# Kernel tuning notes

Hardware: AMD Instinct MI355X
Metric: run time of the kernel (lower is better)

## Reference

```python
import jax, jax.numpy as jnp
import numpy as np

B, NE, NN, L = 64, 256, 1024, 512
F_IN, HID = 128, 128
VOCAB = 50000
ALPHA = 0.2
NEG = -9.0e15


def _leaky(z):
    return jnp.where(z >= 0, z, ALPHA * z)


def hga_layer(x, adj, W, W2, W3, a, a2, wc, transfer, concat):
    # x: [B, NN, Fin], adj: [B, NE, NN] (hyperedge incidence)
    O = W2.shape[1]
    x4 = x @ W2                      # [B, NN, O]
    if transfer:
        x = x @ W                    # [B, NN, O]
    # node->edge attention: score depends only on node k (query is shared word_context)
    s0 = wc[0] @ a[:O, 0]            # scalar
    e1 = _leaky(x4 @ a[O:, 0] + s0)  # [B, NN]
    e1 = jnp.broadcast_to(e1[:, None, :], adj.shape)          # [B, NE, NN]
    att_edge = jax.nn.softmax(jnp.where(adj > 0, e1, NEG), axis=2)
    edge = att_edge @ x              # [B, NE, O]
    edge4 = edge @ W3                # [B, NE, O]
    # edge->node attention: query = node feat x4[k], key = edge feat edge4[j]
    e2 = _leaky((x4 @ a2[:O, 0])[:, None, :] + (edge4 @ a2[O:, 0])[:, :, None])  # [B, NE, NN]
    att_node = jax.nn.softmax(jnp.where(adj > 0, e2, NEG).transpose(0, 2, 1), axis=2)  # [B, NN, NE]
    node = att_node @ edge           # [B, NN, O]
    return jax.nn.elu(node) if concat else node


def setup_inputs() -> dict:
    key = jax.random.key(0)
    ks = jax.random.split(key, 16)
    stdv = 1.0 / np.sqrt(HID)
    u = lambda k, shape: jax.random.uniform(k, shape, jnp.float32, -stdv, stdv)
    inp = {
        "items": jax.random.randint(ks[0], (B, NN), 0, VOCAB),
        "alias_inputs": jax.random.randint(ks[1], (B, L), 0, NN),
        "node_masks": jnp.ones((B, L), jnp.float32),
        "adj": jax.random.randint(ks[2], (B, NE, NN), 0, 2).astype(jnp.float32),
        "emb": jax.random.normal(ks[3], (VOCAB, F_IN), jnp.float32),
        # layer 1 (transfer=False, concat=True)
        "w2_1": u(ks[4], (F_IN, HID)),
        "w3_1": u(ks[5], (HID, HID)),
        "a_1": u(ks[6], (2 * HID, 1)),
        "a2_1": u(ks[7], (2 * HID, 1)),
        "wc_1": u(ks[8], (1, HID)),
        # layer 2 (transfer=True, concat=False)
        "w_2": u(ks[9], (HID, HID)),
        "w2_2": u(ks[10], (HID, HID)),
        "w3_2": u(ks[11], (HID, HID)),
        "a_2": u(ks[12], (2 * HID, 1)),
        "a2_2": u(ks[13], (2 * HID, 1)),
        "wc_2": u(ks[14], (1, HID)),
        "ln_g": jnp.ones((HID,), jnp.float32),
        "ln_b": jnp.zeros((HID,), jnp.float32),
    }
    return inp


def reference(items, alias_inputs, node_masks, adj, emb,
              w2_1, w3_1, a_1, a2_1, wc_1,
              w_2, w2_2, w3_2, a_2, a2_2, wc_2,
              ln_g, ln_b):
    hidden = emb[items]                                        # [B, NN, F]
    x = hga_layer(hidden, adj, None, w2_1, w3_1, a_1, a2_1, wc_1,
                  transfer=False, concat=True)
    x = hga_layer(x, adj, w_2, w2_2, w3_2, a_2, a2_2, wc_2,
                  transfer=True, concat=False)                 # [B, NN, HID]
    seq = jnp.take_along_axis(x, alias_inputs[:, :, None], axis=1)  # [B, L, HID]
    m = node_masks[:, :, None]
    h = seq * m
    b = jnp.sum(h * m, axis=-2) / jnp.sum(node_masks, -1, keepdims=True)  # [B, HID]
    mu = jnp.mean(b, -1, keepdims=True)
    var = jnp.mean((b - mu) ** 2, -1, keepdims=True)
    return (b - mu) / jnp.sqrt(var + 1e-6) * ln_g + ln_b
```

## Files before the change

kernel.cpp:

```cpp
#include <hip/hip_runtime.h>
#include <hip/hip_bf16.h>

typedef __hip_bfloat16 bf16;
typedef __attribute__((ext_vector_type(8))) unsigned short u16x8;
typedef __attribute__((ext_vector_type(4))) unsigned short u16x4;
typedef __attribute__((ext_vector_type(4))) float f32x4;
typedef __attribute__((ext_vector_type(8))) short bf16x8;

#define B_   64
#define NE_  256
#define NN_  1024
#define L_   512
#define HID_ 128
#define ALPHA_ 0.2f

__device__ __forceinline__ float bfu(unsigned short u){
  unsigned int x = ((unsigned int)u) << 16;
  union { unsigned int i; float f; } c; c.i = x; return c.f;
}
__device__ __forceinline__ unsigned short f2b(float f){
  bf16 h = __float2bfloat16(f);
  union { bf16 b; unsigned short u; } c; c.b = h; return c.u;
}
__device__ __forceinline__ int swz(int r, int c){ return (c ^ (r & 3) ^ ((r >> 2) & 3)) & 3; }

__global__ void k_small(const float* __restrict__ w2_1, const float* __restrict__ w3_1,
                        const float* __restrict__ a_1,  const float* __restrict__ a2_1,
                        const float* __restrict__ wc_1,
                        const float* __restrict__ w2_2, const float* __restrict__ w3_2,
                        const float* __restrict__ a_2,  const float* __restrict__ a2_2,
                        const float* __restrict__ wc_2,
                        const float* __restrict__ w_2,
                        const int* __restrict__ alias, const float* __restrict__ masks,
                        float* __restrict__ consts, unsigned short* __restrict__ W2T,
                        float* __restrict__ wcount, float* __restrict__ msum,
                        float* __restrict__ pooled)
{
  __shared__ float wcs[1024];
  __shared__ float red4[4];
  int blk = blockIdx.x, t = threadIdx.x;
  if (blk < 6) {
    if (t < 128) {
      const float* M; const float* v;
      switch (blk) {
        case 0: M = w2_1; v = a_1  + 128; break;
        case 1: M = w2_1; v = a2_1;       break;
        case 2: M = w3_1; v = a2_1 + 128; break;
        case 3: M = w2_2; v = a_2  + 128; break;
        case 4: M = w2_2; v = a2_2;       break;
        default: M = w3_2; v = a2_2 + 128; break;
      }
      float acc = 0.f;
      #pragma unroll 4
      for (int o = 0; o < 128; o += 4) {
        f32x4 m = *(const f32x4*)(M + t*128 + o);
        f32x4 x = *(const f32x4*)(v + o);
        acc += m[0]*x[0] + m[1]*x[1] + m[2]*x[2] + m[3]*x[3];
      }
      consts[blk*128 + t] = acc;
    }
  } else if (blk < 8) {
    const float* wc = (blk == 6) ? wc_1 : wc_2;
    const float* a  = (blk == 6) ? a_1  : a_2;
    if (t < 64) {
      float s = wc[t]*a[t] + wc[t+64]*a[t+64];
      #pragma unroll
      for (int sh = 32; sh > 0; sh >>= 1) s += __shfl_xor(s, sh);
      if (t == 0) consts[768 + (blk - 6)] = s;
    }
  } else if (blk == 8) {
    if (t < 128) for (int k = 0; k < 128; ++k) W2T[t*128 + k] = f2b(w_2[k*128 + t]);
  } else if (blk == 9) {
    for (int i = t; i < B_*HID_; i += 256) pooled[i] = 0.f;
  } else {
    int b = blk - 10;
    #pragma unroll
    for (int j = 0; j < 4; ++j) wcs[t + j*256] = 0.f;
    __syncthreads();
    float s = 0.f;
    #pragma unroll
    for (int j = 0; j < 2; ++j) {
      int l = t + j*256;
      float m = masks[b*L_ + l];
      int idx = alias[b*L_ + l];
      atomicAdd(&wcs[idx], m*m);
      s += m;
    }
    #pragma unroll
    for (int sh = 32; sh > 0; sh >>= 1) s += __shfl_xor(s, sh);
    if ((t & 63) == 0) red4[t >> 6] = s;
    __syncthreads();
    if (t == 0) msum[b] = red4[0] + red4[1] + red4[2] + red4[3];
    #pragma unroll
    for (int j = 0; j < 4; ++j) wcount[(long)b*NN_ + t + j*256] = wcs[t + j*256];
  }
}

__global__ __launch_bounds__(256) void k_prep(
    const float* __restrict__ adj,
    unsigned long long* __restrict__ ADJBb,
    unsigned short* __restrict__ ADJT16)
{
  __shared__ unsigned long long Lbits[16][17];
  const int id = blockIdx.x;
  const int b  = id & 63;
  const int ec = id >> 6;
  const int t  = threadIdx.x;
  const int wv = t >> 6, lane = t & 63;
  const int grp = lane >> 4;
  const int gl  = lane & 15;

  #pragma unroll
  for (int rr = 0; rr < 4; ++rr) {
    const int r = wv*4 + rr;
    const int e = ec*16 + r;
    const float* src = adj + ((long)b*NE_ + e)*NN_;
    #pragma unroll
    for (int i = 0; i < 4; ++i) {
      f32x4 v = *(const f32x4*)(src + i*256 + lane*4);
      unsigned long long nib =
            (unsigned long long)(v[0] != 0.f)
          | ((unsigned long long)(v[1] != 0.f) << 1)
          | ((unsigned long long)(v[2] != 0.f) << 2)
          | ((unsigned long long)(v[3] != 0.f) << 3);
      unsigned long long word = nib << (gl * 4);
      #pragma unroll
      for (int s = 1; s < 16; s <<= 1)
        word |= __shfl_xor(word, s);
      if (gl == 0) {
        Lbits[r][i*4 + grp] = word;
        ADJBb[((long)b*NE_ + e)*16 + i*4 + grp] = word;
      }
    }
  }
  __syncthreads();
  #pragma unroll
  for (int j = 0; j < 4; ++j) {
    int n = t + 256*j;
    int w = n >> 6, bitn = n & 63;
    unsigned int o = 0;
    #pragma unroll
    for (int rr = 0; rr < 16; ++rr)
      o |= (unsigned int)((Lbits[rr][w] >> bitn) & 1ull) << rr;
    ADJT16[((long)b*NN_ + n)*16 + ec] = (unsigned short)o;
  }
}

__global__ void k_fproj(const float* __restrict__ emb, const int* __restrict__ gitems,
                        const float* __restrict__ consts,
                        float* __restrict__ w1, float* __restrict__ f1,
                        unsigned short* __restrict__ YT)
{
  __shared__ float ce1s[128], cf1s[128];
  __shared__ __attribute__((aligned(16))) unsigned short T[64][132];
  int b = blockIdx.y, n0 = blockIdx.x * 64, t = threadIdx.x;
  if (t < 128) { ce1s[t] = consts[t]; cf1s[t] = consts[128 + t]; }
  __syncthreads();
  int r = t >> 2, h0 = (t & 3) * 32;
  long row = (long)b*NN_ + n0 + r;
  float s0 = consts[768];
  float xv[32];
  const float* sp = emb + (long)gitems[row]*HID_ + h0;
  #pragma unroll
  for (int j = 0; j < 32; j += 4) {
    f32x4 v = *(const f32x4*)(sp + j);
    #pragma unroll
    for (int k = 0; k < 4; ++k) xv[j+k] = v[k];
  }
  float p1 = 0.f, p2 = 0.f;
  #pragma unroll
  for (int j = 0; j < 32; ++j) { p1 += xv[j]*ce1s[h0+j]; p2 += xv[j]*cf1s[h0+j]; }
  p1 += __shfl_xor(p1, 1, 4); p1 += __shfl_xor(p1, 2, 4);
  p2 += __shfl_xor(p2, 1, 4); p2 += __shfl_xor(p2, 2, 4);
  float z = p1 + s0; z = (z >= 0.f) ? z : ALPHA_*z;
  float w = __expf(z);
  if ((t & 3) == 0) { w1[row] = w; f1[row] = p2; }
  #pragma unroll
  for (int j = 0; j < 32; j += 4) {
    u16x4 o;
    #pragma unroll
    for (int k = 0; k < 4; ++k) o[k] = f2b(w * xv[j+k]);
    *(u16x4*)&T[r][h0+j] = o;
  }
  __syncthreads();
  int h = t >> 1, nh = (t & 1) * 32;
  unsigned short* dst = YT + ((long)b*HID_ + h)*NN_ + n0 + nh;
  #pragma unroll
  for (int j = 0; j < 32; j += 8) {
    u16x8 o;
    #pragma unroll
    for (int k = 0; k < 8; ++k) o[k] = T[nh+j+k][h];
    *(u16x8*)&dst[j] = o;
  }
}

template<int TRANSFER>
__global__ __launch_bounds__(256) void k_gemm_edge(
    const unsigned char* __restrict__ ADJ8,
    const unsigned short* __restrict__ YT,
    const float* __restrict__ w1v,
    const float* __restrict__ consts, int layer,
    const unsigned short* __restrict__ W2T,
    unsigned short* __restrict__ ET,
    float* __restrict__ f2o)
{
  __shared__ __attribute__((aligned(16))) unsigned short SM[12288];
  __shared__ float dsum[64];
  const int id = blockIdx.x;
  const int b = id & 63;
  const long e0 = (long)(id >> 6) * 64;
  const int t = threadIdx.x;
  const int lane = t & 63;
  const int w = t >> 6, wm = w >> 1, wn = w & 1;
  const int r4 = t >> 2, c4 = t & 3;
  const int lr = lane & 15, g = lane >> 4;

  f32x4 acc[2][4];
  #pragma unroll
  for (int i = 0; i < 2; ++i)
    #pragma unroll
    for (int j = 0; j < 4; ++j) acc[i][j] = (f32x4){0.f,0.f,0.f,0.f};

  const unsigned char*  Ab = ADJ8 + ((long)b*NE_ + e0 + r4)*(NN_ >> 3);
  const unsigned short* Bb = YT + (long)b*HID_*NN_;
  const float*          wb = w1v + (long)b*NN_;

  unsigned int ab; u16x8 bv0, bv1; f32x4 wv0, wv1;
  float dot = 0.f;

  auto stage = [&](int kc) {
    ab  = Ab[(kc >> 3) + c4];
    wv0 = *(const f32x4*)(wb + kc + c4*8);
    wv1 = *(const f32x4*)(wb + kc + c4*8 + 4);
    bv0 = *(const u16x8*)(Bb + (long)r4*NN_ + kc + c4*8);
    bv1 = *(const u16x8*)(Bb + (long)(64+r4)*NN_ + kc + c4*8);
  };
  auto commit = [&](int buf) {
    u16x8 av;
    #pragma unroll
    for (int j = 0; j < 8; ++j) {
      unsigned int bit = (ab >> j) & 1u;
      av[j] = bit ? (unsigned short)0x3F80 : (unsigned short)0;
      float wj = (j < 4) ? wv0[j] : wv1[j-4];
      dot += bit ? wj : 0.f;
    }
    *(u16x8*)&SM[buf*2048 + r4*32 + swz(r4,c4)*8] = av;
    *(u16x8*)&SM[4096 + buf*4096 + r4*32 + swz(r4,c4)*8] = bv0;
    *(u16x8*)&SM[4096 + buf*4096 + (64+r4)*32 + swz(64+r4,c4)*8] = bv1;
  };

  stage(0); commit(0);
  int cur = 0;
  const int NIT = NN_/32;
  for (int it = 0; it < NIT; ++it) {
    __syncthreads();
    if (it+1 < NIT) stage((it+1)*32);
    const unsigned short* AsB = &SM[cur*2048];
    const unsigned short* BsB = &SM[4096 + cur*4096];
    bf16x8 af[2], bfr[4];
    #pragma unroll
    for (int mt = 0; mt < 2; ++mt) {
      int r = wm*32 + mt*16 + lr;
      af[mt] = *(const bf16x8*)&AsB[r*32 + swz(r,g)*8];
    }
    #pragma unroll
    for (int nt = 0; nt < 4; ++nt) {
      int n = wn*64 + nt*16 + lr;
      bfr[nt] = *(const bf16x8*)&BsB[n*32 + swz(n,g)*8];
    }
    #pragma unroll
    for (int mt = 0; mt < 2; ++mt)
      #pragma unroll
      for (int nt = 0; nt < 4; ++nt)
        acc[mt][nt] = __builtin_amdgcn_mfma_f32_16x16x32_bf16(af[mt], bfr[nt], acc[mt][nt], 0, 0, 0);
    if (it+1 < NIT) { commit(cur^1); cur ^= 1; }
  }
  dot += __shfl_down(dot, 2, 4); dot += __shfl_down(dot, 1, 4);
  if ((lane & 3) == 0) dsum[r4] = dot;
  __syncthreads();
  #pragma unroll
  for (int mt = 0; mt < 2; ++mt)
    #pragma unroll
    for (int nt = 0; nt < 4; ++nt) {
      int col = wn*64 + nt*16 + lr;
      #pragma unroll
      for (int q = 0; q < 4; ++q) {
        int rl = wm*32 + mt*16 + g*4 + q;
        SM[rl*136 + col] = f2b(acc[mt][nt][q] / dsum[rl]);
      }
    }
  __syncthreads();
  if (TRANSFER) {
    f32x4 acc2[2][4];
    #pragma unroll
    for (int i = 0; i < 2; ++i)
      #pragma unroll
      for (int j = 0; j < 4; ++j) acc2[i][j] = (f32x4){0.f,0.f,0.f,0.f};
    #pragma unroll
    for (int kc2 = 0; kc2 < 4; ++kc2) {
      bf16x8 af[2], bfr[4];
      #pragma unroll
      for (int mt = 0; mt < 2; ++mt) {
        int r = wm*32 + mt*16 + lr;
        af[mt] = *(const bf16x8*)&SM[r*136 + kc2*32 + g*8];
      }
      #pragma unroll
      for (int nt = 0; nt < 4; ++nt) {
        int n = wn*64 + nt*16 + lr;
        bfr[nt] = *(const bf16x8*)(W2T + n*128 + kc2*32 + g*8);
      }
      #pragma unroll
      for (int mt = 0; mt < 2; ++mt)
        #pragma unroll
        for (int nt = 0; nt < 4; ++nt)
          acc2[mt][nt] = __builtin_amdgcn_mfma_f32_16x16x32_bf16(af[mt], bfr[nt], acc2[mt][nt], 0, 0, 0);
    }
    __syncthreads();
    #pragma unroll
    for (int mt = 0; mt < 2; ++mt)
      #pragma unroll
      for (int nt = 0; nt < 4; ++nt) {
        int col = wn*64 + nt*16 + lr;
        #pragma unroll
        for (int q = 0; q < 4; ++q) {
          int rl = wm*32 + mt*16 + g*4 + q;
          SM[rl*136 + col] = f2b(acc2[mt][nt][q]);
        }
      }
    __syncthreads();
  }
  {
    const float* cf2 = consts + layer*384 + 256;
    int r = t >> 2, h0 = (t & 3) * 32;
    float p = 0.f;
    #pragma unroll
    for (int j = 0; j < 32; ++j) p += bfu(SM[r*136 + h0 + j]) * cf2[h0 + j];
    p += __shfl_down(p, 2, 4); p += __shfl_down(p, 1, 4);
    if ((t & 3) == 0) f2o[(long)b*NE_ + e0 + r] = p;
  }
  {
    int h = t >> 1, eh = (t & 1) * 32;
    unsigned short* dst = ET + ((long)b*HID_ + h)*NE_ + e0 + eh;
    #pragma unroll
    for (int j = 0; j < 32; j += 8) {
      u16x8 o;
      #pragma unroll
      for (int k = 0; k < 8; ++k) o[k] = SM[(eh+j+k)*136 + h];
      *(u16x8*)&dst[j] = o;
    }
  }
}

template<int EPI>
__global__ __launch_bounds__(256, 2) void k_gemm_att(
    const unsigned char* __restrict__ ADJ8,
    const unsigned short* __restrict__ ET,
    const float* __restrict__ f1v, const float* __restrict__ f2v,
    const float* __restrict__ consts,
    unsigned short* __restrict__ YTout, float* __restrict__ w1o, float* __restrict__ f1o,
    const float* __restrict__ wcount, float* __restrict__ pooled)
{
  __shared__ __attribute__((aligned(16))) unsigned short SM[12288];
  __shared__ float dsum[64];
  __shared__ float colsum[128];
  __shared__ float wrow[64];
  const int id = blockIdx.x;
  const int b = id & 63;
  const long m0 = (long)(id >> 6) * 64;
  const int t = threadIdx.x;
  const int lane = t & 63;
  const int w = t >> 6, wm = w >> 1, wn = w & 1;
  const int r4 = t >> 2, c4 = t & 3;
  const int lr = lane & 15, g = lane >> 4;

  f32x4 acc[2][4];
  #pragma unroll
  for (int i = 0; i < 2; ++i)
    #pragma unroll
    for (int j = 0; j < 4; ++j) acc[i][j] = (f32x4){0.f,0.f,0.f,0.f};

  const float f1r = f1v[(long)b*NN_ + m0 + r4];
  const unsigned char*  Ab = ADJ8 + ((long)b*NN_ + m0 + r4)*(NE_ >> 3);
  const unsigned short* Bb = ET + (long)b*HID_*NE_;
  const float* f2p = f2v + (long)b*NE_;

  unsigned int ab; u16x8 bv0, bv1; f32x4 fv0, fv1;
  float dot = 0.f;

  auto stage = [&](int kc) {
    ab  = Ab[(kc >> 3) + c4];
    fv0 = *(const f32x4*)(f2p + kc + c4*8);
    fv1 = *(const f32x4*)(f2p + kc + c4*8 + 4);
    bv0 = *(const u16x8*)(Bb + (long)r4*NE_ + kc + c4*8);
    bv1 = *(const u16x8*)(Bb + (long)(64+r4)*NE_ + kc + c4*8);
  };
  auto commit = [&](int buf) {
    u16x8 av;
    #pragma unroll
    for (int j = 0; j < 8; ++j) {
      unsigned int bit = (ab >> j) & 1u;
      float z = f1r + ((j < 4) ? fv0[j] : fv1[j-4]);
      z = (z >= 0.f) ? z : ALPHA_ * z;
      float wt = bit ? __expf(z) : 0.f;
      unsigned short us = f2b(wt);
      av[j] = us; dot += bfu(us);
    }
    *(u16x8*)&SM[buf*2048 + r4*32 + swz(r4,c4)*8] = av;
    *(u16x8*)&SM[4096 + buf*4096 + r4*32 + swz(r4,c4)*8] = bv0;
    *(u16x8*)&SM[4096 + buf*4096 + (64+r4)*32 + swz(64+r4,c4)*8] = bv1;
  };

  stage(0); commit(0);
  int cur = 0;
  const int NIT = NE_/32;
  for (int it = 0; it < NIT; ++it) {
    __syncthreads();
    if (it+1 < NIT) stage((it+1)*32);
    const unsigned short* AsB = &SM[cur*2048];
    const unsigned short* BsB = &SM[4096 + cur*4096];
    bf16x8 af[2], bfr[4];
    #pragma unroll
    for (int mt = 0; mt < 2; ++mt) {
      int r = wm*32 + mt*16 + lr;
      af[mt] = *(const bf16x8*)&AsB[r*32 + swz(r,g)*8];
    }
    #pragma unroll
    for (int nt = 0; nt < 4; ++nt) {
      int n = wn*64 + nt*16 + lr;
      bfr[nt] = *(const bf16x8*)&BsB[n*32 + swz(n,g)*8];
    }
    #pragma unroll
    for (int mt = 0; mt < 2; ++mt)
      #pragma unroll
      for (int nt = 0; nt < 4; ++nt)
        acc[mt][nt] = __builtin_amdgcn_mfma_f32_16x16x32_bf16(af[mt], bfr[nt], acc[mt][nt], 0, 0, 0);
    if (it+1 < NIT) { commit(cur^1); cur ^= 1; }
  }
  dot += __shfl_down(dot, 2, 4); dot += __shfl_down(dot, 1, 4);
  if ((lane & 3) == 0) dsum[r4] = dot;
  if (EPI == 2 && t < 128) colsum[t] = 0.f;
  __syncthreads();

  if (EPI == 1) {
    #pragma unroll
    for (int mt = 0; mt < 2; ++mt)
      #pragma unroll
      for (int nt = 0; nt < 4; ++nt) {
        int col = wn*64 + nt*16 + lr;
        #pragma unroll
        for (int q = 0; q < 4; ++q) {
          int rl = wm*32 + mt*16 + g*4 + q;
          float v = acc[mt][nt][q] / dsum[rl];
          v = (v > 0.f) ? v : expm1f(v);
          SM[rl*136 + col] = f2b(v);
        }
      }
    __syncthreads();
    {
      const float* ce1 = consts + 384;
      const float* cf1 = consts + 512;
      int r = t >> 2, h0 = (t & 3) * 32;
      float p1 = 0.f, p2 = 0.f;
      #pragma unroll
      for (int j = 0; j < 32; ++j) {
        float xv = bfu(SM[r*136 + h0 + j]);
        p1 += xv * ce1[h0 + j];
        p2 += xv * cf1[h0 + j];
      }
      p1 += __shfl_down(p1, 2, 4); p1 += __shfl_down(p1, 1, 4);
      p2 += __shfl_down(p2, 2, 4); p2 += __shfl_down(p2, 1, 4);
      if ((t & 3) == 0) {
        float z = p1 + consts[769];
        z = (z >= 0.f) ? z : ALPHA_ * z;
        float wv = __expf(z);
        wrow[r] = wv;
        w1o[(long)b*NN_ + m0 + r] = wv;
        f1o[(long)b*NN_ + m0 + r] = p2;
      }
    }
    __syncthreads();
    {
      int h = t >> 1, nh = (t & 1) * 32;
      unsigned short* dst = YTout + ((long)b*HID_ + h)*NN_ + m0 + nh;
      #pragma unroll
      for (int j = 0; j < 32; j += 8) {
        u16x8 o;
        #pragma unroll
        for (int k = 0; k < 8; ++k) {
          int rr = nh + j + k;
          o[k] = f2b(wrow[rr] * bfu(SM[rr*136 + h]));
        }
        *(u16x8*)&dst[j] = o;
      }
    }
  } else {
    float psum[4] = {0.f, 0.f, 0.f, 0.f};
    #pragma unroll
    for (int mt = 0; mt < 2; ++mt)
      #pragma unroll
      for (int q = 0; q < 4; ++q) {
        int rl = wm*32 + mt*16 + g*4 + q;
        float wc = wcount[(long)b*NN_ + m0 + rl];
        float inv = wc / dsum[rl];
        #pragma unroll
        for (int nt = 0; nt < 4; ++nt) psum[nt] += inv * acc[mt][nt][q];
      }
    #pragma unroll
    for (int nt = 0; nt < 4; ++nt) atomicAdd(&colsum[wn*64 + nt*16 + lr], psum[nt]);
    __syncthreads();
    if (t < 128) atomicAdd(&pooled[(long)b*HID_ + t], colsum[t]);
  }
}

__global__ void k_ln(const float* __restrict__ pooled, const float* __restrict__ msum,
                     const float* __restrict__ ln_g, const float* __restrict__ ln_b,
                     float* __restrict__ out)
{
  int b = blockIdx.x, t = threadIdx.x;
  __shared__ float sr[2];
  float bv = pooled[b*HID_ + t] / msum[b];
  int lane = t & 63;
  float p = bv;
  #pragma unroll
  for (int s = 32; s > 0; s >>= 1) p += __shfl_xor(p, s);
  if (lane == 0) sr[t >> 6] = p;
  __syncthreads();
  float mu = (sr[0] + sr[1]) * (1.f / HID_);
  float dv = bv - mu;
  p = dv * dv;
  #pragma unroll
  for (int s = 32; s > 0; s >>= 1) p += __shfl_xor(p, s);
  __syncthreads();
  if (lane == 0) sr[t >> 6] = p;
  __syncthreads();
  float var = (sr[0] + sr[1]) * (1.f / HID_);
  out[b*HID_ + t] = dv / sqrtf(var + 1e-6f) * ln_g[t] + ln_b[t];
}

extern "C" void kernel_launch(void* const* d_in, const int* in_sizes, int n_in,
                              void* d_out, int out_size, void* d_ws, size_t ws_size,
                              hipStream_t stream)
{
  const int*   items = (const int*)d_in[0];
  const int*   alias = (const int*)d_in[1];
  const float* masks = (const float*)d_in[2];
  const float* adj   = (const float*)d_in[3];
  const float* emb   = (const float*)d_in[4];
  const float* w2_1  = (const float*)d_in[5];
  const float* w3_1  = (const float*)d_in[6];
  const float* a_1   = (const float*)d_in[7];
  const float* a2_1  = (const float*)d_in[8];
  const float* wc_1  = (const float*)d_in[9];
  const float* w_2   = (const float*)d_in[10];
  const float* w2_2  = (const float*)d_in[11];
  const float* w3_2  = (const float*)d_in[12];
  const float* a_2   = (const float*)d_in[13];
  const float* a2_2  = (const float*)d_in[14];
  const float* wc_2  = (const float*)d_in[15];
  const float* ln_g  = (const float*)d_in[16];
  const float* ln_b  = (const float*)d_in[17];
  float* out = (float*)d_out;

  char* ws = (char*)d_ws;
  size_t off = 0;
  auto alloc = [&](size_t bytes) -> void* {
    void* p = ws + off; off += (bytes + 255) / 256 * 256; return p;
  };
  unsigned long long* ADJBb = (unsigned long long*)alloc((size_t)B_*NE_*(NN_/8));
  unsigned short*     ADJT16= (unsigned short*)    alloc((size_t)B_*NN_*(NE_/8));
  unsigned short* YT   = (unsigned short*)alloc((size_t)B_*HID_*NN_*2);
  unsigned short* ET   = (unsigned short*)alloc((size_t)B_*HID_*NE_*2);
  float* wcount= (float*)alloc((size_t)B_*NN_*4);
  float* pooled= (float*)alloc((size_t)B_*HID_*4);
  float* w1L1  = (float*)alloc((size_t)B_*NN_*4);
  float* f1L1  = (float*)alloc((size_t)B_*NN_*4);
  float* w1L2  = (float*)alloc((size_t)B_*NN_*4);
  float* f1L2  = (float*)alloc((size_t)B_*NN_*4);
  float* f2    = (float*)alloc((size_t)B_*NE_*4);
  float* msum  = (float*)alloc(B_*4);
  float* consts= (float*)alloc(772*4);
  unsigned short* W2T = (unsigned short*)alloc((size_t)HID_*HID_*2);
  if (off > ws_size) return;

  k_small<<<74, 256, 0, stream>>>(w2_1, w3_1, a_1, a2_1, wc_1, w2_2, w3_2, a_2, a2_2, wc_2,
                                  w_2, alias, masks, consts, W2T, wcount, msum, pooled);
  k_prep<<<B_*16, 256, 0, stream>>>(adj, ADJBb, ADJT16);
  k_fproj<<<dim3(NN_/64, B_), 256, 0, stream>>>(emb, items, consts, w1L1, f1L1, YT);

  k_gemm_edge<0><<<B_*(NE_/64), 256, 0, stream>>>((const unsigned char*)ADJBb, YT, w1L1,
        consts, 0, W2T, ET, f2);
  k_gemm_att<1><<<B_*(NN_/64), 256, 0, stream>>>((const unsigned char*)ADJT16, ET, f1L1, f2,
        consts, YT, w1L2, f1L2, nullptr, nullptr);

  k_gemm_edge<1><<<B_*(NE_/64), 256, 0, stream>>>((const unsigned char*)ADJBb, YT, w1L2,
        consts, 1, W2T, ET, f2);
  k_gemm_att<2><<<B_*(NN_/64), 256, 0, stream>>>((const unsigned char*)ADJT16, ET, f1L2, f2,
        consts, nullptr, nullptr, nullptr, wcount, pooled);

  k_ln<<<B_, HID_, 0, stream>>>(pooled, msum, ln_g, ln_b, out);
}
```

Measured before the change: 129.4 us.

## Merge front-end kernels into one launch and fuse layernorm into last attention kernel

Combines the small-constants, adjacency bit-packing and first-layer feature projection kernels into a single grid. The projection blocks recompute the projection constants locally, so they no longer depend on the constants kernel. The final layernorm kernel is removed: the last block finishing each batch row in the final attention kernel, found through an atomic counter, performs the normalization. This cuts two kernel launches and the inter-kernel gaps, at the cost of redundant per-block constant computation and a threadfence plus atomic per block.

```diff
diff --git a/kernel.cpp b/kernel.cpp
--- a/kernel.cpp
+++ b/kernel.cpp
@@ -24,173 +24,192 @@
 }
 __device__ __forceinline__ int swz(int r, int c){ return (c ^ (r & 3) ^ ((r >> 2) & 3)) & 3; }
 
-__global__ void k_small(const float* __restrict__ w2_1, const float* __restrict__ w3_1,
-                        const float* __restrict__ a_1,  const float* __restrict__ a2_1,
-                        const float* __restrict__ wc_1,
-                        const float* __restrict__ w2_2, const float* __restrict__ w3_2,
-                        const float* __restrict__ a_2,  const float* __restrict__ a2_2,
-                        const float* __restrict__ wc_2,
-                        const float* __restrict__ w_2,
-                        const int* __restrict__ alias, const float* __restrict__ masks,
-                        float* __restrict__ consts, unsigned short* __restrict__ W2T,
-                        float* __restrict__ wcount, float* __restrict__ msum,
-                        float* __restrict__ pooled)
+__global__ __launch_bounds__(256) void k_front(
+    const float* __restrict__ adj,
+    unsigned long long* __restrict__ ADJBb, unsigned short* __restrict__ ADJT16,
+    const float* __restrict__ emb, const int* __restrict__ items,
+    const float* __restrict__ w2_1, const float* __restrict__ w3_1,
+    const float* __restrict__ a_1,  const float* __restrict__ a2_1,
+    const float* __restrict__ wc_1,
+    const float* __restrict__ w_2,
+    const float* __restrict__ w2_2, const float* __restrict__ w3_2,
+    const float* __restrict__ a_2,  const float* __restrict__ a2_2,
+    const float* __restrict__ wc_2,
+    const int* __restrict__ alias, const float* __restrict__ masks,
+    float* __restrict__ w1L1, float* __restrict__ f1L1,
+    unsigned short* __restrict__ YT,
+    float* __restrict__ consts, unsigned short* __restrict__ W2T,
+    float* __restrict__ wcount, float* __restrict__ msum,
+    float* __restrict__ pooled, int* __restrict__ lncnt)
 {
-  __shared__ float wcs[1024];
-  __shared__ float red4[4];
-  int blk = blockIdx.x, t = threadIdx.x;
-  if (blk < 6) {
-    if (t < 128) {
-      const float* M; const float* v;
-      switch (blk) {
-        case 0: M = w2_1; v = a_1  + 128; break;
-        case 1: M = w2_1; v = a2_1;       break;
-        case 2: M = w3_1; v = a2_1 + 128; break;
-        case 3: M = w2_2; v = a_2  + 128; break;
-        case 4: M = w2_2; v = a2_2;       break;
-        default: M = w3_2; v = a2_2 + 128; break;
-      }
+  __shared__ __attribute__((aligned(16))) unsigned char SMEM[18944];
+  const int id = blockIdx.x;
+  const int t  = threadIdx.x;
+
+  if (id < 1024) {
+    unsigned long long (*Lbits)[17] = (unsigned long long(*)[17])SMEM;
+    const int b  = id & 63;
+    const int ec = id >> 6;
+    const int wv = t >> 6, lane = t & 63;
+    const int grp = lane >> 4;
+    const int gl  = lane & 15;
+    #pragma unroll
+    for (int rr = 0; rr < 4; ++rr) {
+      const int r = wv*4 + rr;
+      const int e = ec*16 + r;
+      const float* src = adj + ((long)b*NE_ + e)*NN_;
+      #pragma unroll
+      for (int i = 0; i < 4; ++i) {
+        f32x4 v = *(const f32x4*)(src + i*256 + lane*4);
+        unsigned long long nib =
+              (unsigned long long)(v[0] != 0.f)
+            | ((unsigned long long)(v[1] != 0.f) << 1)
+            | ((unsigned long long)(v[2] != 0.f) << 2)
+            | ((unsigned long long)(v[3] != 0.f) << 3);
+        unsigned long long word = nib << (gl * 4);
+        #pragma unroll
+        for (int s = 1; s < 16; s <<= 1)
+          word |= __shfl_xor(word, s);
+        if (gl == 0) {
+          Lbits[r][i*4 + grp] = word;
+          ADJBb[((long)b*NE_ + e)*16 + i*4 + grp] = word;
+        }
+      }
+    }
+    __syncthreads();
+    #pragma unroll
+    for (int j = 0; j < 4; ++j) {
+      int n = t + 256*j;
+      int w = n >> 6, bitn = n & 63;
+      unsigned int o = 0;
+      #pragma unroll
+      for (int rr = 0; rr < 16; ++rr)
+        o |= (unsigned int)((Lbits[rr][w] >> bitn) & 1ull) << rr;
+      ADJT16[((long)b*NN_ + n)*16 + ec] = (unsigned short)o;
+    }
+  } else if (id < 2048) {
+    float* ce1s = (float*)SMEM;
+    float* cf1s = (float*)(SMEM + 512);
+    float* s0s  = (float*)(SMEM + 1024);
+    unsigned short (*T)[132] = (unsigned short(*)[132])(SMEM + 1056);
+    {
+      int rr = t & 127;
+      const float* Mrow = w2_1 + rr*128;
+      const float* vv = (t < 128) ? (a_1 + 128) : a2_1;
       float acc = 0.f;
       #pragma unroll 4
       for (int o = 0; o < 128; o += 4) {
-        f32x4 m = *(const f32x4*)(M + t*128 + o);
-        f32x4 x = *(const f32x4*)(v + o);
+        f32x4 m = *(const f32x4*)(Mrow + o);
+        f32x4 x = *(const f32x4*)(vv + o);
         acc += m[0]*x[0] + m[1]*x[1] + m[2]*x[2] + m[3]*x[3];
       }
-      consts[blk*128 + t] = acc;
-    }
-  } else if (blk < 8) {
-    const float* wc = (blk == 6) ? wc_1 : wc_2;
-    const float* a  = (blk == 6) ? a_1  : a_2;
-    if (t < 64) {
-      float s = wc[t]*a[t] + wc[t+64]*a[t+64];
+      if (t < 128) ce1s[rr] = acc; else cf1s[rr] = acc;
+      if (t < 64) {
+        float s = wc_1[t]*a_1[t] + wc_1[t+64]*a_1[t+64];
+        #pragma unroll
+        for (int sh = 32; sh > 0; sh >>= 1) s += __shfl_xor(s, sh);
+        if (t == 0) s0s[0] = s;
+      }
+    }
+    __syncthreads();
+    int fid = id - 1024;
+    int b = fid & 63, n0 = (fid >> 6) * 64;
+    int r = t >> 2, h0 = (t & 3) * 32;
+    long row = (long)b*NN_ + n0 + r;
+    float s0 = s0s[0];
+    float xv[32];
+    const float* sp = emb + (long)items[row]*HID_ + h0;
+    #pragma unroll
+    for (int j = 0; j < 32; j += 4) {
+      f32x4 v = *(const f32x4*)(sp + j);
+      #pragma unroll
+      for (int k = 0; k < 4; ++k) xv[j+k] = v[k];
+    }
+    float p1 = 0.f, p2 = 0.f;
+    #pragma unroll
+    for (int j = 0; j < 32; ++j) { p1 += xv[j]*ce1s[h0+j]; p2 += xv[j]*cf1s[h0+j]; }
+    p1 += __shfl_xor(p1, 1, 4); p1 += __shfl_xor(p1, 2, 4);
+    p2 += __shfl_xor(p2, 1, 4); p2 += __shfl_xor(p2, 2, 4);
+    float z = p1 + s0; z = (z >= 0.f) ? z : ALPHA_*z;
+    float w = __expf(z);
+    if ((t & 3) == 0) { w1L1[row] = w; f1L1[row] = p2; }
+    #pragma unroll
+    for (int j = 0; j < 32; j += 4) {
+      u16x4 o;
+      #pragma unroll
+      for (int k = 0; k < 4; ++k) o[k] = f2b(w * xv[j+k]);
+      *(u16x4*)&T[r][h0+j] = o;
+    }
+    __syncthreads();
+    int h = t >> 1, nh = (t & 1) * 32;
+    unsigned short* dst = YT + ((long)b*HID_ + h)*NN_ + n0 + nh;
+    #pragma unroll
+    for (int j = 0; j < 32; j += 8) {
+      u16x8 o;
+      #pragma unroll
+      for (int k = 0; k < 8; ++k) o[k] = T[nh+j+k][h];
+      *(u16x8*)&dst[j] = o;
+    }
+  } else {
+    int blk = id - 2048;
+    float* wcs  = (float*)SMEM;
+    float* red4 = (float*)(SMEM + 4096);
+    if (blk < 6) {
+      if (t < 128) {
+        const float* M; const float* v;
+        switch (blk) {
+          case 0: M = w2_1; v = a_1  + 128; break;
+          case 1: M = w2_1; v = a2_1;       break;
+          case 2: M = w3_1; v = a2_1 + 128; break;
+          case 3: M = w2_2; v = a_2  + 128; break;
+          case 4: M = w2_2; v = a2_2;       break;
+          default: M = w3_2; v = a2_2 + 128; break;
+        }
+        float acc = 0.f;
+        #pragma unroll 4
+        for (int o = 0; o < 128; o += 4) {
+          f32x4 m = *(const f32x4*)(M + t*128 + o);
+          f32x4 x = *(const f32x4*)(v + o);
+          acc += m[0]*x[0] + m[1]*x[1] + m[2]*x[2] + m[3]*x[3];
+        }
+        consts[blk*128 + t] = acc;
+      }
+    } else if (blk < 8) {
+      const float* wc = (blk == 6) ? wc_1 : wc_2;
+      const float* a  = (blk == 6) ? a_1  : a_2;
+      if (t < 64) {
+        float s = wc[t]*a[t] + wc[t+64]*a[t+64];
+        #pragma unroll
+        for (int sh = 32; sh > 0; sh >>= 1) s += __shfl_xor(s, sh);
+        if (t == 0) consts[768 + (blk - 6)] = s;
+      }
+    } else if (blk == 8) {
+      if (t < 128) for (int k = 0; k < 128; ++k) W2T[t*128 + k] = f2b(w_2[k*128 + t]);
+    } else if (blk == 9) {
+      for (int i = t; i < B_*HID_; i += 256) pooled[i] = 0.f;
+      if (t < 64) lncnt[t] = 0;
+    } else {
+      int b = blk - 10;
+      #pragma unroll
+      for (int j = 0; j < 4; ++j) wcs[t + j*256] = 0.f;
+      __syncthreads();
+      float s = 0.f;
+      #pragma unroll
+      for (int j = 0; j < 2; ++j) {
+        int l = t + j*256;
+        float m = masks[b*L_ + l];
+        int idx = alias[b*L_ + l];
+        atomicAdd(&wcs[idx], m*m);
+        s += m;
+      }
       #pragma unroll
       for (int sh = 32; sh > 0; sh >>= 1) s += __shfl_xor(s, sh);
-      if (t == 0) consts[768 + (blk - 6)] = s;
-    }
-  } else if (blk == 8) {
-    if (t < 128) for (int k = 0; k < 128; ++k) W2T[t*128 + k] = f2b(w_2[k*128 + t]);
-  } else if (blk == 9) {
-    for (int i = t; i < B_*HID_; i += 256) pooled[i] = 0.f;
-  } else {
-    int b = blk - 10;
-    #pragma unroll
-    for (int j = 0; j < 4; ++j) wcs[t + j*256] = 0.f;
-    __syncthreads();
-    float s = 0.f;
-    #pragma unroll
-    for (int j = 0; j < 2; ++j) {
-      int l = t + j*256;
-      float m = masks[b*L_ + l];
-      int idx = alias[b*L_ + l];
-      atomicAdd(&wcs[idx], m*m);
-      s += m;
-    }
-    #pragma unroll
-    for (int sh = 32; sh > 0; sh >>= 1) s += __shfl_xor(s, sh);
-    if ((t & 63) == 0) red4[t >> 6] = s;
-    __syncthreads();
-    if (t == 0) msum[b] = red4[0] + red4[1] + red4[2] + red4[3];
-    #pragma unroll
-    for (int j = 0; j < 4; ++j) wcount[(long)b*NN_ + t + j*256] = wcs[t + j*256];
-  }
-}
-
-__global__ __launch_bounds__(256) void k_prep(
-    const float* __restrict__ adj,
-    unsigned long long* __restrict__ ADJBb,
-    unsigned short* __restrict__ ADJT16)
-{
-  __shared__ unsigned long long Lbits[16][17];
-  const int id = blockIdx.x;
-  const int b  = id & 63;
-  const int ec = id >> 6;
-  const int t  = threadIdx.x;
-  const int wv = t >> 6, lane = t & 63;
-  const int grp = lane >> 4;
-  const int gl  = lane & 15;
-
-  #pragma unroll
-  for (int rr = 0; rr < 4; ++rr) {
-    const int r = wv*4 + rr;
-    const int e = ec*16 + r;
-    const float* src = adj + ((long)b*NE_ + e)*NN_;
-    #pragma unroll
-    for (int i = 0; i < 4; ++i) {
-      f32x4 v = *(const f32x4*)(src + i*256 + lane*4);
-      unsigned long long nib =
-            (unsigned long long)(v[0] != 0.f)
-          | ((unsigned long long)(v[1] != 0.f) << 1)
-          | ((unsigned long long)(v[2] != 0.f) << 2)
-          | ((unsigned long long)(v[3] != 0.f) << 3);
-      unsigned long long word = nib << (gl * 4);
-      #pragma unroll
-      for (int s = 1; s < 16; s <<= 1)
-        word |= __shfl_xor(word, s);
-      if (gl == 0) {
-        Lbits[r][i*4 + grp] = word;
-        ADJBb[((long)b*NE_ + e)*16 + i*4 + grp] = word;
-      }
-    }
-  }
-  __syncthreads();
-  #pragma unroll
-  for (int j = 0; j < 4; ++j) {
-    int n = t + 256*j;
-    int w = n >> 6, bitn = n & 63;
-    unsigned int o = 0;
-    #pragma unroll
-    for (int rr = 0; rr < 16; ++rr)
-      o |= (unsigned int)((Lbits[rr][w] >> bitn) & 1ull) << rr;
-    ADJT16[((long)b*NN_ + n)*16 + ec] = (unsigned short)o;
-  }
-}
-
-__global__ void k_fproj(const float* __restrict__ emb, const int* __restrict__ gitems,
-                        const float* __restrict__ consts,
-                        float* __restrict__ w1, float* __restrict__ f1,
-                        unsigned short* __restrict__ YT)
-{
-  __shared__ float ce1s[128], cf1s[128];
-  __shared__ __attribute__((aligned(16))) unsigned short T[64][132];
-  int b = blockIdx.y, n0 = blockIdx.x * 64, t = threadIdx.x;
-  if (t < 128) { ce1s[t] = consts[t]; cf1s[t] = consts[128 + t]; }
-  __syncthreads();
-  int r = t >> 2, h0 = (t & 3) * 32;
-  long row = (long)b*NN_ + n0 + r;
-  float s0 = consts[768];
-  float xv[32];
-  const float* sp = emb + (long)gitems[row]*HID_ + h0;
-  #pragma unroll
-  for (int j = 0; j < 32; j += 4) {
-    f32x4 v = *(const f32x4*)(sp + j);
-    #pragma unroll
-    for (int k = 0; k < 4; ++k) xv[j+k] = v[k];
-  }
-  float p1 = 0.f, p2 = 0.f;
-  #pragma unroll
-  for (int j = 0; j < 32; ++j) { p1 += xv[j]*ce1s[h0+j]; p2 += xv[j]*cf1s[h0+j]; }
-  p1 += __shfl_xor(p1, 1, 4); p1 += __shfl_xor(p1, 2, 4);
-  p2 += __shfl_xor(p2, 1, 4); p2 += __shfl_xor(p2, 2, 4);
-  float z = p1 + s0; z = (z >= 0.f) ? z : ALPHA_*z;
-  float w = __expf(z);
-  if ((t & 3) == 0) { w1[row] = w; f1[row] = p2; }
-  #pragma unroll
-  for (int j = 0; j < 32; j += 4) {
-    u16x4 o;
-    #pragma unroll
-    for (int k = 0; k < 4; ++k) o[k] = f2b(w * xv[j+k]);
-    *(u16x4*)&T[r][h0+j] = o;
-  }
-  __syncthreads();
-  int h = t >> 1, nh = (t & 1) * 32;
-  unsigned short* dst = YT + ((long)b*HID_ + h)*NN_ + n0 + nh;
-  #pragma unroll
-  for (int j = 0; j < 32; j += 8) {
-    u16x8 o;
-    #pragma unroll
-    for (int k = 0; k < 8; ++k) o[k] = T[nh+j+k][h];
-    *(u16x8*)&dst[j] = o;
+      if ((t & 63) == 0) red4[t >> 6] = s;
+      __syncthreads();
+      if (t == 0) msum[b] = red4[0] + red4[1] + red4[2] + red4[3];
+      #pragma unroll
+      for (int j = 0; j < 4; ++j) wcount[(long)b*NN_ + t + j*256] = wcs[t + j*256];
+    }
   }
 }
 
@@ -358,12 +377,16 @@
     const float* __restrict__ f1v, const float* __restrict__ f2v,
     const float* __restrict__ consts,
     unsigned short* __restrict__ YTout, float* __restrict__ w1o, float* __restrict__ f1o,
-    const float* __restrict__ wcount, float* __restrict__ pooled)
+    const float* __restrict__ wcount, float* __restrict__ pooled,
+    const float* __restrict__ msum, const float* __restrict__ ln_g,
+    const float* __restrict__ ln_b, float* __restrict__ outp, int* __restrict__ lncnt)
 {
   __shared__ __attribute__((aligned(16))) unsigned short SM[12288];
   __shared__ float dsum[64];
   __shared__ float colsum[128];
   __shared__ float wrow[64];
+  __shared__ int lastF;
+  __shared__ float sr2[2];
   const int id = blockIdx.x;
   const int b = id & 63;
   const long m0 = (long)(id >> 6) * 64;
@@ -509,32 +532,30 @@
     for (int nt = 0; nt < 4; ++nt) atomicAdd(&colsum[wn*64 + nt*16 + lr], psum[nt]);
     __syncthreads();
     if (t < 128) atomicAdd(&pooled[(long)b*HID_ + t], colsum[t]);
+    __threadfence();
+    __syncthreads();
+    if (t == 0) lastF = (atomicAdd(&lncnt[b], 1) == (NN_/64) - 1);
+    __syncthreads();
+    if (lastF) {
+      float bv = 0.f;
+      if (t < 128) bv = atomicAdd(&pooled[(long)b*HID_ + t], 0.f) / msum[b];
+      float p = bv;
+      #pragma unroll
+      for (int s = 32; s > 0; s >>= 1) p += __shfl_xor(p, s);
+      if (t < 128 && (t & 63) == 0) sr2[t >> 6] = p;
+      __syncthreads();
+      float mu = (sr2[0] + sr2[1]) * (1.f / HID_);
+      float dv = bv - mu;
+      p = dv * dv;
+      #pragma unroll
+      for (int s = 32; s > 0; s >>= 1) p += __shfl_xor(p, s);
+      __syncthreads();
+      if (t < 128 && (t & 63) == 0) sr2[t >> 6] = p;
+      __syncthreads();
+      float var = (sr2[0] + sr2[1]) * (1.f / HID_);
+      if (t < 128) outp[b*HID_ + t] = dv / sqrtf(var + 1e-6f) * ln_g[t] + ln_b[t];
+    }
   }
-}
-
-__global__ void k_ln(const float* __restrict__ pooled, const float* __restrict__ msum,
-                     const float* __restrict__ ln_g, const float* __restrict__ ln_b,
-                     float* __restrict__ out)
-{
-  int b = blockIdx.x, t = threadIdx.x;
-  __shared__ float sr[2];
-  float bv = pooled[b*HID_ + t] / msum[b];
-  int lane = t & 63;
-  float p = bv;
-  #pragma unroll
-  for (int s = 32; s > 0; s >>= 1) p += __shfl_xor(p, s);
-  if (lane == 0) sr[t >> 6] = p;
-  __syncthreads();
-  float mu = (sr[0] + sr[1]) * (1.f / HID_);
-  float dv = bv - mu;
-  p = dv * dv;
-  #pragma unroll
-  for (int s = 32; s > 0; s >>= 1) p += __shfl_xor(p, s);
-  __syncthreads();
-  if (lane == 0) sr[t >> 6] = p;
-  __syncthreads();
-  float var = (sr[0] + sr[1]) * (1.f / HID_);
-  out[b*HID_ + t] = dv / sqrtf(var + 1e-6f) * ln_g[t] + ln_b[t];
 }
 
 extern "C" void kernel_launch(void* const* d_in, const int* in_sizes, int n_in,
@@ -580,22 +601,21 @@
   float* msum  = (float*)alloc(B_*4);
   float* consts= (float*)alloc(772*4);
   unsigned short* W2T = (unsigned short*)alloc((size_t)HID_*HID_*2);
+  int*   lncnt = (int*)alloc(B_*4);
   if (off > ws_size) return;
 
-  k_small<<<74, 256, 0, stream>>>(w2_1, w3_1, a_1, a2_1, wc_1, w2_2, w3_2, a_2, a2_2, wc_2,
-                                  w_2, alias, masks, consts, W2T, wcount, msum, pooled);
-  k_prep<<<B_*16, 256, 0, stream>>>(adj, ADJBb, ADJT16);
-  k_fproj<<<dim3(NN_/64, B_), 256, 0, stream>>>(emb, items, consts, w1L1, f1L1, YT);
+  k_front<<<2122, 256, 0, stream>>>(adj, ADJBb, ADJT16, emb, items,
+        w2_1, w3_1, a_1, a2_1, wc_1, w_2, w2_2, w3_2, a_2, a2_2, wc_2,
+        alias, masks, w1L1, f1L1, YT, consts, W2T, wcount, msum, pooled, lncnt);
 
   k_gemm_edge<0><<<B_*(NE_/64), 256, 0, stream>>>((const unsigned char*)ADJBb, YT, w1L1,
         consts, 0, W2T, ET, f2);
   k_gemm_att<1><<<B_*(NN_/64), 256, 0, stream>>>((const unsigned char*)ADJT16, ET, f1L1, f2,
-        consts, YT, w1L2, f1L2, nullptr, nullptr);
+        consts, YT, w1L2, f1L2, nullptr, nullptr, nullptr, nullptr, nullptr, nullptr, nullptr);
 
   k_gemm_edge<1><<<B_*(NE_/64), 256, 0, stream>>>((const unsigned char*)ADJBb, YT, w1L2,
         consts, 1, W2T, ET, f2);
   k_gemm_att<2><<<B_*(NN_/64), 256, 0, stream>>>((const unsigned char*)ADJT16, ET, f1L2, f2,
-        consts, nullptr, nullptr, nullptr, wcount, pooled);
-
-  k_ln<<<B_, HID_, 0, stream>>>(pooled, msum, ln_g, ln_b, out);
+        consts, nullptr, nullptr, nullptr, wcount, pooled,
+        msum, ln_g, ln_b, out, lncnt);
 }
```

Result: slower. 187.8 us (+45.1%).
